# Performance work log

Measured on AMD Instinct MI355X. Metric: run time of the kernel, lower is better.

The kernel has to match this reference:

```python
import jax, jax.numpy as jnp
import numpy as np

NUM_HEADS = 32
HIDDEN = 4096
HEAD_DIM = HIDDEN // NUM_HEADS
BATCH = 1
SEQ = 2048


def setup_inputs() -> dict:
    key = jax.random.key(0)
    ks = jax.random.split(key, 8)
    hidden_states = jax.random.normal(ks[0], (BATCH, SEQ, HIDDEN), dtype=jnp.float32)
    residual = jax.random.normal(ks[1], (BATCH, SEQ, HIDDEN), dtype=jnp.float32)
    # BLOOM alibi: [batch*heads, 1, kv_len], broadcast over q_length in baddbmm
    alibi = jax.random.normal(ks[2], (BATCH * NUM_HEADS, 1, SEQ), dtype=jnp.float32) * 0.1
    # causal boolean mask: True = masked (filled with -inf before softmax)
    attention_mask = ~jnp.tril(jnp.ones((SEQ, SEQ), dtype=bool))[None, None, :, :]
    scale = 0.02
    Wqkv = jax.random.normal(ks[3], (3 * HIDDEN, HIDDEN), dtype=jnp.float32) * scale
    bqkv = jax.random.normal(ks[4], (3 * HIDDEN,), dtype=jnp.float32) * scale
    Wd = jax.random.normal(ks[5], (HIDDEN, HIDDEN), dtype=jnp.float32) * scale
    bd = jax.random.normal(ks[6], (HIDDEN,), dtype=jnp.float32) * scale
    return {"hidden_states": hidden_states, "residual": residual, "alibi": alibi,
            "attention_mask": attention_mask, "Wqkv": Wqkv, "bqkv": bqkv,
            "Wd": Wd, "bd": bd}


def reference(hidden_states, residual, alibi, attention_mask, Wqkv, bqkv, Wd, bd):
    B, S, H = hidden_states.shape
    nh, hd = NUM_HEADS, HEAD_DIM
    inv_norm = 1.0 / np.sqrt(hd).astype(np.float32)

    # fused QKV projection, BLOOM interleaved layout [B, S, nh, 3, hd]
    fused = hidden_states @ Wqkv.T + bqkv           # [B, S, 3H]
    fused = fused.reshape(B, S, nh, 3, hd)
    q = jnp.transpose(fused[..., 0, :], (0, 2, 1, 3))  # [B, nh, S, hd]
    k = jnp.transpose(fused[..., 1, :], (0, 2, 1, 3))  # [B, nh, S, hd]
    v = jnp.transpose(fused[..., 2, :], (0, 2, 1, 3))  # [B, nh, S, hd]

    # baddbmm: alibi + inv_norm * Q @ K^T
    alibi_b = alibi.reshape(B, nh, 1, S)                # broadcast over q_length
    scores = alibi_b + inv_norm * jnp.einsum('bhqd,bhkd->bhqk', q, k)
    scores = jnp.where(attention_mask, jnp.finfo(scores.dtype).min, scores)
    probs = jax.nn.softmax(scores, axis=-1)             # [B, nh, S, S]

    ctx = jnp.einsum('bhqk,bhkd->bhqd', probs, v)       # [B, nh, S, hd]
    ctx = jnp.transpose(ctx, (0, 2, 1, 3)).reshape(B, S, H)
    out = ctx @ Wd.T + bd
    return residual + out
```

## Files before the change

### kernel.cpp

```cpp
#include <hip/hip_runtime.h>


#define SEQL 2048
#define HIDN 4096
#define NHEAD 32
#define HDIM 128
#define H3 12288

typedef __bf16 bf16x8 __attribute__((ext_vector_type(8)));
typedef float f32x4 __attribute__((ext_vector_type(4)));
typedef unsigned short u16x8 __attribute__((ext_vector_type(8)));
typedef unsigned int u32x4 __attribute__((ext_vector_type(4)));

__device__ __forceinline__ unsigned short f2bf(float f) {
  union { float f; unsigned u; } v; v.f = f;
  return (unsigned short)((v.u + 0x7FFFu + ((v.u >> 16) & 1u)) >> 16);
}

__device__ __forceinline__ unsigned cvtpk(float lo, float hi) {
  unsigned r;
  asm("v_cvt_pk_bf16_f32 %0, %1, %2" : "=v"(r) : "v"(lo), "v"(hi));
  return r;
}

__device__ __forceinline__ void gload_lds16(const void* g, void* l) {
  __builtin_amdgcn_global_load_lds(
      (const __attribute__((address_space(1))) void*)g,
      (__attribute__((address_space(3))) void*)l, 16, 0, 0);
}

__global__ __launch_bounds__(256) void cvt_f32_bf16(
    const float* __restrict__ in, unsigned short* __restrict__ out, long long n) {
  long long i = ((long long)blockIdx.x * blockDim.x + threadIdx.x) * 8;
  long long stride = (long long)gridDim.x * blockDim.x * 8;
  for (; i < n; i += stride) {
    float4 a = *(const float4*)(in + i);
    float4 b = *(const float4*)(in + i + 4);
    u16x8 o;
    o[0] = f2bf(a.x); o[1] = f2bf(a.y); o[2] = f2bf(a.z); o[3] = f2bf(a.w);
    o[4] = f2bf(b.x); o[5] = f2bf(b.y); o[6] = f2bf(b.z); o[7] = f2bf(b.w);
    *(u16x8*)(out + i) = o;
  }
}

template <int EPI>
__global__ __launch_bounds__(256) void gemm_nt(
    const unsigned short* __restrict__ A, const unsigned short* __restrict__ B,
    int M, int N, int K,
    const float* __restrict__ bias, const float* __restrict__ residual,
    float* __restrict__ outf,
    unsigned short* __restrict__ q_bf, unsigned short* __restrict__ k_bf,
    unsigned short* __restrict__ v_t) {
  __shared__ unsigned short As[128 * 64];
  __shared__ unsigned short Bs[128 * 64];

  const int tid = threadIdx.x;
  const int l = tid & 63;
  const int w = tid >> 6;
  const int wr = (w >> 1) * 64;
  const int wc = (w & 1) * 64;

  const int nb = gridDim.x;
  const int lin = (blockIdx.x & 7) * (nb >> 3) + (blockIdx.x >> 3);
  const int tm0 = (lin & 15) * 128;
  const int tn0 = (lin >> 4) * 128;

  const int lr = l >> 3;
  const int lc = (l & 7) ^ lr;

  f32x4 acc[4][4] = {};

  for (int kt = 0; kt < K; kt += 64) {
    __syncthreads();
#pragma unroll
    for (int i = 0; i < 4; ++i) {
      const int row = w * 32 + i * 8 + lr;
      gload_lds16(&A[(long long)(tm0 + row) * K + kt + lc * 8],
                  (char*)As + (w * 4 + i) * 1024);
      gload_lds16(&B[(long long)(tn0 + row) * K + kt + lc * 8],
                  (char*)Bs + (w * 4 + i) * 1024);
    }
    __syncthreads();
#pragma unroll
    for (int kk = 0; kk < 2; ++kk) {
      const int colb = kk * 64 + (l >> 4) * 16;
      bf16x8 af[4], bfr[4];
#pragma unroll
      for (int m = 0; m < 4; ++m) {
        int row = wr + m * 16 + (l & 15);
        af[m] = *(const bf16x8*)((char*)As + row * 128 + (colb ^ ((row & 7) << 4)));
      }
#pragma unroll
      for (int n = 0; n < 4; ++n) {
        int row = wc + n * 16 + (l & 15);
        bfr[n] = *(const bf16x8*)((char*)Bs + row * 128 + (colb ^ ((row & 7) << 4)));
      }
#pragma unroll
      for (int m = 0; m < 4; ++m)
#pragma unroll
        for (int n = 0; n < 4; ++n)
          acc[m][n] = __builtin_amdgcn_mfma_f32_16x16x32_bf16(af[m], bfr[n], acc[m][n], 0, 0, 0);
    }
  }

#pragma unroll
  for (int m = 0; m < 4; ++m) {
#pragma unroll
    for (int n = 0; n < 4; ++n) {
      const int col = tn0 + wc + n * 16 + (l & 15);
      const float bv = bias[col];
#pragma unroll
      for (int r = 0; r < 4; ++r) {
        const int rowg = tm0 + wr + m * 16 + (l >> 4) * 4 + r;
        float v = acc[m][n][r] + bv;
        if (EPI == 0) {
          const int head = col / 384;
          const int rem = col - head * 384;
          const int which = rem >> 7;
          const int d = rem & 127;
          const unsigned short bv16 = f2bf(v);
          if (which == 0)
            q_bf[(long long)(head * SEQL + rowg) * HDIM + d] = bv16;
          else if (which == 1)
            k_bf[(long long)(head * SEQL + rowg) * HDIM + d] = bv16;
          else
            v_t[(long long)(head * HDIM + d) * SEQL + rowg] = bv16;
        } else {
          const long long idx = (long long)rowg * N + col;
          outf[idx] = v + residual[idx];
        }
      }
    }
  }
}

__global__ __launch_bounds__(256) void attn_fwd(
    const unsigned short* __restrict__ q_bf, const unsigned short* __restrict__ k_bf,
    const unsigned short* __restrict__ v_t, const float* __restrict__ alibi,
    unsigned short* __restrict__ ctx_bf) {
  __shared__ unsigned short Ks[64 * 128];
  __shared__ unsigned short Vs[128 * 64];
  __shared__ float Al[SEQL];

  const int tid = threadIdx.x;
  const int l = tid & 63;
  const int w = tid >> 6;
  const int q = l & 15;
  const int g = l >> 4;

  const float LOG2E = 1.4426950408889634f;

  const int b = blockIdx.x;
  const int i_ = b >> 3;
  const int h = (b & 7) * 4 + (i_ & 3);
  const int qtile = 31 - (i_ >> 2);
  const int qw = qtile * 64 + w * 16;
  const int qrow = qw + q;
  const int ntiles = qtile + 1;

  for (int i = tid; i < SEQL; i += 256) Al[i] = alibi[h * SEQL + i] * LOG2E;

  bf16x8 qf[4];
  {
    const unsigned short* qp =
        &q_bf[(long long)(h * SEQL + qw + q) * HDIM + g * 8];
#pragma unroll
    for (int kk = 0; kk < 4; ++kk) qf[kk] = *(const bf16x8*)(qp + kk * 32);
  }

  f32x4 oacc[8] = {};
  float mrun = -__builtin_inff();
  float lrun = 0.f;
  const float inv_norm2 = 0.08838834764831845f * 1.4426950408889634f;

  const int kR = l >> 4, kC = l & 15;
  const int vR = l >> 3, vC = (l & 7) ^ vR;

  for (int t = 0; t < ntiles; ++t) {
    const int kv0 = t * 64;
    __syncthreads();
#pragma unroll
    for (int i = 0; i < 4; ++i) {
      const int krow = w * 16 + i * 4 + kR;
      const int ksrc = kC ^ ((i & 1) * 4 + kR);
      gload_lds16(&k_bf[(long long)(h * SEQL + kv0 + krow) * HDIM + ksrc * 8],
                  (char*)Ks + (w * 4 + i) * 1024);
      const int vrow = w * 32 + i * 8 + vR;
      gload_lds16(&v_t[(long long)(h * HDIM + vrow) * SEQL + kv0 + vC * 8],
                  (char*)Vs + (w * 4 + i) * 1024);
    }
    __syncthreads();

    if (kv0 <= qw + 15) {
      f32x4 sacc[4] = {};
#pragma unroll
      for (int kk = 0; kk < 4; ++kk) {
        const int colb = kk * 64 + g * 16;
#pragma unroll
        for (int n = 0; n < 4; ++n) {
          const int row = n * 16 + q;
          bf16x8 kf = *(const bf16x8*)((char*)Ks + row * 256 + (colb ^ ((row & 7) << 4)));
          sacc[n] = __builtin_amdgcn_mfma_f32_16x16x32_bf16(kf, qf[kk], sacc[n], 0, 0, 0);
        }
      }

      float p[4][4];
      float m0 = -__builtin_inff();
#pragma unroll
      for (int n = 0; n < 4; ++n) {
        const f32x4 alv = *(const f32x4*)(Al + kv0 + n * 16 + g * 4);
#pragma unroll
        for (int r = 0; r < 4; ++r) {
          const int kv = kv0 + n * 16 + g * 4 + r;
          float v = alv[r] + inv_norm2 * sacc[n][r];
          v = (kv > qrow) ? -__builtin_inff() : v;
          p[n][r] = v;
          m0 = fmaxf(m0, v);
        }
      }
      m0 = fmaxf(m0, __shfl_xor(m0, 16, 64));
      m0 = fmaxf(m0, __shfl_xor(m0, 32, 64));
      if (__ballot(m0 > mrun + 11.0f)) {
        const float mnew = fmaxf(mrun, m0);
        const float scale = exp2f(mrun - mnew);
        mrun = mnew;
        lrun *= scale;
#pragma unroll
        for (int n2 = 0; n2 < 8; ++n2)
#pragma unroll
          for (int r = 0; r < 4; ++r) oacc[n2][r] *= scale;
      }
      float p0 = 0.f;
#pragma unroll
      for (int n = 0; n < 4; ++n)
#pragma unroll
        for (int r = 0; r < 4; ++r) {
          const float pv = exp2f(p[n][r] - mrun);
          p[n][r] = pv;
          p0 += pv;
        }
      p0 += __shfl_xor(p0, 16, 64);
      p0 += __shfl_xor(p0, 32, 64);
      lrun += p0;

      bf16x8 pb[2];
#pragma unroll
      for (int kk2 = 0; kk2 < 2; ++kk2) {
        const int n0 = 2 * kk2;
        const unsigned pk0 = cvtpk(p[n0][0], p[n0][1]);
        const unsigned pk1 = cvtpk(p[n0][2], p[n0][3]);
        const unsigned pk2 = cvtpk(p[n0 + 1][0], p[n0 + 1][1]);
        const unsigned pk3 = cvtpk(p[n0 + 1][2], p[n0 + 1][3]);
        const int s0 = q + 32 * (g & 1);
        const int s2 = s0 + 16;
        const unsigned a0 = __shfl((int)pk0, s0, 64), b0 = __shfl((int)pk2, s0, 64);
        const unsigned a1 = __shfl((int)pk1, s0, 64), b1 = __shfl((int)pk3, s0, 64);
        const unsigned a2 = __shfl((int)pk0, s2, 64), b2 = __shfl((int)pk2, s2, 64);
        const unsigned a3 = __shfl((int)pk1, s2, 64), b3 = __shfl((int)pk3, s2, 64);
        const bool lo = (g < 2);
        u32x4 wv;
        wv[0] = lo ? a0 : b0; wv[1] = lo ? a1 : b1;
        wv[2] = lo ? a2 : b2; wv[3] = lo ? a3 : b3;
        pb[kk2] = __builtin_bit_cast(bf16x8, wv);
      }

#pragma unroll
      for (int n2 = 0; n2 < 8; ++n2) {
#pragma unroll
        for (int kk2 = 0; kk2 < 2; ++kk2) {
          const int row = n2 * 16 + q;
          const int colb = kk2 * 64 + g * 16;
          bf16x8 vf = *(const bf16x8*)((char*)Vs + row * 128 + (colb ^ ((row & 7) << 4)));
          oacc[n2] = __builtin_amdgcn_mfma_f32_16x16x32_bf16(vf, pb[kk2], oacc[n2], 0, 0, 0);
        }
      }
    }
  }

  __syncthreads();
  {
    char* scr = (char*)Ks + w * 4096;
    const float rdiv = 1.0f / lrun;
#pragma unroll
    for (int n2 = 0; n2 < 8; ++n2)
#pragma unroll
      for (int r = 0; r < 4; ++r) {
        const int d = n2 * 16 + g * 4 + r;
        *(unsigned short*)(scr + ((q * 256 + d * 2) ^ ((q & 7) << 4))) =
            f2bf(oacc[n2][r] * rdiv);
      }
    __threadfence_block();
    const int q2 = l >> 2;
#pragma unroll
    for (int i = 0; i < 4; ++i) {
      const int chunk = (l & 3) + i * 4;
      u16x8 v = *(const u16x8*)(scr + ((q2 * 256 + chunk * 16) ^ ((q2 & 7) << 4)));
      *(u16x8*)&ctx_bf[(long long)(qw + q2) * HIDN + h * HDIM + chunk * 8] = v;
    }
  }
}

extern "C" void kernel_launch(void* const* d_in, const int* in_sizes, int n_in,
                              void* d_out, int out_size, void* d_ws, size_t ws_size,
                              hipStream_t stream) {
  const float* hidden = (const float*)d_in[0];
  const float* residual = (const float*)d_in[1];
  const float* alibi = (const float*)d_in[2];
  const float* Wqkv = (const float*)d_in[4];
  const float* bqkv = (const float*)d_in[5];
  const float* Wd = (const float*)d_in[6];
  const float* bd = (const float*)d_in[7];
  float* out = (float*)d_out;

  char* ws = (char*)d_ws;
  const size_t MB16 = 16777216;
  unsigned short* q_bf = (unsigned short*)(ws);
  unsigned short* k_bf = (unsigned short*)(ws + MB16);
  unsigned short* v_t = (unsigned short*)(ws + 2 * MB16);
  unsigned short* hid_bf = (unsigned short*)(ws + 3 * MB16);
  unsigned short* wqkv_bf = (unsigned short*)(ws + 4 * MB16);
  unsigned short* wd_bf = (unsigned short*)(ws + 4 * MB16);
  unsigned short* ctx_bf = (unsigned short*)(ws + 4 * MB16 + 33554432);

  cvt_f32_bf16<<<4096, 256, 0, stream>>>(hidden, hid_bf, (long long)SEQL * HIDN);
  cvt_f32_bf16<<<24576, 256, 0, stream>>>(Wqkv, wqkv_bf, (long long)H3 * HIDN);

  gemm_nt<0><<<(SEQL / 128) * (H3 / 128), 256, 0, stream>>>(
      hid_bf, wqkv_bf, SEQL, H3, HIDN, bqkv, nullptr, nullptr, q_bf, k_bf, v_t);

  cvt_f32_bf16<<<8192, 256, 0, stream>>>(Wd, wd_bf, (long long)HIDN * HIDN);

  attn_fwd<<<NHEAD * (SEQL / 64), 256, 0, stream>>>(q_bf, k_bf, v_t, alibi, ctx_bf);

  gemm_nt<1><<<(SEQL / 128) * (HIDN / 128), 256, 0, stream>>>(
      ctx_bf, wd_bf, SEQL, HIDN, HIDN, bd, residual, out, nullptr, nullptr, nullptr);
}
```

Before: 475.8 us.

## Process two 16-row query groups per wave to double K/V tile reuse

The attention kernel now assigns 128 query rows per block (32 per wave, as two 16-row groups) instead of 64. Each K/V tile loaded into LDS and each K/V fragment read from LDS feeds twice as many MFMAs, which halves global K/V traffic and the number of barrier-separated loads per unit of work. The cost is more registers per wave (doubled accumulators and Q fragments), which may lower occupancy. It also halves the grid size, which can worsen load balance given the causal triangular work distribution.

```diff
diff --git a/kernel.cpp b/kernel.cpp
--- a/kernel.cpp
+++ b/kernel.cpp
@@ -146,31 +146,31 @@
   const int l = tid & 63;
   const int w = tid >> 6;
   const int q = l & 15;
-  const int g = l >> 4;
+  const int lg = l >> 4;
 
   const float LOG2E = 1.4426950408889634f;
 
   const int b = blockIdx.x;
   const int i_ = b >> 3;
   const int h = (b & 7) * 4 + (i_ & 3);
-  const int qtile = 31 - (i_ >> 2);
-  const int qw = qtile * 64 + w * 16;
-  const int qrow = qw + q;
-  const int ntiles = qtile + 1;
-
-  for (int i = tid; i < SEQL; i += 256) Al[i] = alibi[h * SEQL + i] * LOG2E;
-
-  bf16x8 qf[4];
-  {
+  const int qtile = 15 - (i_ >> 2);
+  const int qw = qtile * 128 + w * 32;
+  const int ntiles = 2 * qtile + 2;
+
+  for (int i = tid; i < ntiles * 64; i += 256) Al[i] = alibi[h * SEQL + i] * LOG2E;
+
+  bf16x8 qf[2][4];
+#pragma unroll
+  for (int g = 0; g < 2; ++g) {
     const unsigned short* qp =
-        &q_bf[(long long)(h * SEQL + qw + q) * HDIM + g * 8];
-#pragma unroll
-    for (int kk = 0; kk < 4; ++kk) qf[kk] = *(const bf16x8*)(qp + kk * 32);
-  }
-
-  f32x4 oacc[8] = {};
-  float mrun = -__builtin_inff();
-  float lrun = 0.f;
+        &q_bf[(long long)(h * SEQL + qw + g * 16 + q) * HDIM + lg * 8];
+#pragma unroll
+    for (int kk = 0; kk < 4; ++kk) qf[g][kk] = *(const bf16x8*)(qp + kk * 32);
+  }
+
+  f32x4 oacc[2][8] = {};
+  float mrun[2] = {-__builtin_inff(), -__builtin_inff()};
+  float lrun[2] = {0.f, 0.f};
   const float inv_norm2 = 0.08838834764831845f * 1.4426950408889634f;
 
   const int kR = l >> 4, kC = l & 15;
@@ -181,87 +181,93 @@
     __syncthreads();
 #pragma unroll
     for (int i = 0; i < 4; ++i) {
-      const int krow = w * 16 + i * 4 + kR;
+      const int c = w * 4 + i;
+      const int krow = c * 4 + kR;
       const int ksrc = kC ^ ((i & 1) * 4 + kR);
       gload_lds16(&k_bf[(long long)(h * SEQL + kv0 + krow) * HDIM + ksrc * 8],
-                  (char*)Ks + (w * 4 + i) * 1024);
-      const int vrow = w * 32 + i * 8 + vR;
+                  (char*)Ks + c * 1024);
+      const int vrow = c * 8 + vR;
       gload_lds16(&v_t[(long long)(h * HDIM + vrow) * SEQL + kv0 + vC * 8],
-                  (char*)Vs + (w * 4 + i) * 1024);
+                  (char*)Vs + c * 1024);
     }
     __syncthreads();
 
-    if (kv0 <= qw + 15) {
-      f32x4 sacc[4] = {};
+    if (kv0 <= qw + 31) {
+      f32x4 sacc[2][4] = {};
 #pragma unroll
       for (int kk = 0; kk < 4; ++kk) {
-        const int colb = kk * 64 + g * 16;
+        const int colb = kk * 64 + lg * 16;
 #pragma unroll
         for (int n = 0; n < 4; ++n) {
           const int row = n * 16 + q;
           bf16x8 kf = *(const bf16x8*)((char*)Ks + row * 256 + (colb ^ ((row & 7) << 4)));
-          sacc[n] = __builtin_amdgcn_mfma_f32_16x16x32_bf16(kf, qf[kk], sacc[n], 0, 0, 0);
-        }
-      }
-
-      float p[4][4];
-      float m0 = -__builtin_inff();
-#pragma unroll
-      for (int n = 0; n < 4; ++n) {
-        const f32x4 alv = *(const f32x4*)(Al + kv0 + n * 16 + g * 4);
-#pragma unroll
-        for (int r = 0; r < 4; ++r) {
-          const int kv = kv0 + n * 16 + g * 4 + r;
-          float v = alv[r] + inv_norm2 * sacc[n][r];
-          v = (kv > qrow) ? -__builtin_inff() : v;
-          p[n][r] = v;
-          m0 = fmaxf(m0, v);
-        }
-      }
-      m0 = fmaxf(m0, __shfl_xor(m0, 16, 64));
-      m0 = fmaxf(m0, __shfl_xor(m0, 32, 64));
-      if (__ballot(m0 > mrun + 11.0f)) {
-        const float mnew = fmaxf(mrun, m0);
-        const float scale = exp2f(mrun - mnew);
-        mrun = mnew;
-        lrun *= scale;
-#pragma unroll
-        for (int n2 = 0; n2 < 8; ++n2)
-#pragma unroll
-          for (int r = 0; r < 4; ++r) oacc[n2][r] *= scale;
-      }
-      float p0 = 0.f;
-#pragma unroll
-      for (int n = 0; n < 4; ++n)
-#pragma unroll
-        for (int r = 0; r < 4; ++r) {
-          const float pv = exp2f(p[n][r] - mrun);
-          p[n][r] = pv;
-          p0 += pv;
-        }
-      p0 += __shfl_xor(p0, 16, 64);
-      p0 += __shfl_xor(p0, 32, 64);
-      lrun += p0;
-
-      bf16x8 pb[2];
-#pragma unroll
-      for (int kk2 = 0; kk2 < 2; ++kk2) {
-        const int n0 = 2 * kk2;
-        const unsigned pk0 = cvtpk(p[n0][0], p[n0][1]);
-        const unsigned pk1 = cvtpk(p[n0][2], p[n0][3]);
-        const unsigned pk2 = cvtpk(p[n0 + 1][0], p[n0 + 1][1]);
-        const unsigned pk3 = cvtpk(p[n0 + 1][2], p[n0 + 1][3]);
-        const int s0 = q + 32 * (g & 1);
-        const int s2 = s0 + 16;
-        const unsigned a0 = __shfl((int)pk0, s0, 64), b0 = __shfl((int)pk2, s0, 64);
-        const unsigned a1 = __shfl((int)pk1, s0, 64), b1 = __shfl((int)pk3, s0, 64);
-        const unsigned a2 = __shfl((int)pk0, s2, 64), b2 = __shfl((int)pk2, s2, 64);
-        const unsigned a3 = __shfl((int)pk1, s2, 64), b3 = __shfl((int)pk3, s2, 64);
-        const bool lo = (g < 2);
-        u32x4 wv;
-        wv[0] = lo ? a0 : b0; wv[1] = lo ? a1 : b1;
-        wv[2] = lo ? a2 : b2; wv[3] = lo ? a3 : b3;
-        pb[kk2] = __builtin_bit_cast(bf16x8, wv);
+          sacc[0][n] = __builtin_amdgcn_mfma_f32_16x16x32_bf16(kf, qf[0][kk], sacc[0][n], 0, 0, 0);
+          sacc[1][n] = __builtin_amdgcn_mfma_f32_16x16x32_bf16(kf, qf[1][kk], sacc[1][n], 0, 0, 0);
+        }
+      }
+
+      bf16x8 pb[2][2];
+#pragma unroll
+      for (int g = 0; g < 2; ++g) {
+        const int qrow = qw + g * 16 + q;
+        float p[4][4];
+        float m0 = -__builtin_inff();
+#pragma unroll
+        for (int n = 0; n < 4; ++n) {
+          const f32x4 alv = *(const f32x4*)(Al + kv0 + n * 16 + lg * 4);
+#pragma unroll
+          for (int r = 0; r < 4; ++r) {
+            const int kv = kv0 + n * 16 + lg * 4 + r;
+            float v = alv[r] + inv_norm2 * sacc[g][n][r];
+            v = (kv > qrow) ? -__builtin_inff() : v;
+            p[n][r] = v;
+            m0 = fmaxf(m0, v);
+          }
+        }
+        m0 = fmaxf(m0, __shfl_xor(m0, 16, 64));
+        m0 = fmaxf(m0, __shfl_xor(m0, 32, 64));
+        if (__ballot(m0 > mrun[g] + 11.0f)) {
+          const float mnew = fmaxf(mrun[g], m0);
+          const float scale = exp2f(mrun[g] - mnew);
+          mrun[g] = mnew;
+          lrun[g] *= scale;
+#pragma unroll
+          for (int n2 = 0; n2 < 8; ++n2)
+#pragma unroll
+            for (int r = 0; r < 4; ++r) oacc[g][n2][r] *= scale;
+        }
+        float p0 = 0.f;
+#pragma unroll
+        for (int n = 0; n < 4; ++n)
+#pragma unroll
+          for (int r = 0; r < 4; ++r) {
+            const float pv = exp2f(p[n][r] - mrun[g]);
+            p[n][r] = pv;
+            p0 += pv;
+          }
+        p0 += __shfl_xor(p0, 16, 64);
+        p0 += __shfl_xor(p0, 32, 64);
+        lrun[g] += p0;
+
+#pragma unroll
+        for (int kk2 = 0; kk2 < 2; ++kk2) {
+          const int n0 = 2 * kk2;
+          const unsigned pk0 = cvtpk(p[n0][0], p[n0][1]);
+          const unsigned pk1 = cvtpk(p[n0][2], p[n0][3]);
+          const unsigned pk2 = cvtpk(p[n0 + 1][0], p[n0 + 1][1]);
+          const unsigned pk3 = cvtpk(p[n0 + 1][2], p[n0 + 1][3]);
+          const int s0 = q + 32 * (lg & 1);
+          const int s2 = s0 + 16;
+          const unsigned a0 = __shfl((int)pk0, s0, 64), b0 = __shfl((int)pk2, s0, 64);
+          const unsigned a1 = __shfl((int)pk1, s0, 64), b1 = __shfl((int)pk3, s0, 64);
+          const unsigned a2 = __shfl((int)pk0, s2, 64), b2 = __shfl((int)pk2, s2, 64);
+          const unsigned a3 = __shfl((int)pk1, s2, 64), b3 = __shfl((int)pk3, s2, 64);
+          const bool lo = (lg < 2);
+          u32x4 wv;
+          wv[0] = lo ? a0 : b0; wv[1] = lo ? a1 : b1;
+          wv[2] = lo ? a2 : b2; wv[3] = lo ? a3 : b3;
+          pb[g][kk2] = __builtin_bit_cast(bf16x8, wv);
+        }
       }
 
 #pragma unroll
@@ -269,9 +275,10 @@
 #pragma unroll
         for (int kk2 = 0; kk2 < 2; ++kk2) {
           const int row = n2 * 16 + q;
-          const int colb = kk2 * 64 + g * 16;
+          const int colb = kk2 * 64 + lg * 16;
           bf16x8 vf = *(const bf16x8*)((char*)Vs + row * 128 + (colb ^ ((row & 7) << 4)));
-          oacc[n2] = __builtin_amdgcn_mfma_f32_16x16x32_bf16(vf, pb[kk2], oacc[n2], 0, 0, 0);
+          oacc[0][n2] = __builtin_amdgcn_mfma_f32_16x16x32_bf16(vf, pb[0][kk2], oacc[0][n2], 0, 0, 0);
+          oacc[1][n2] = __builtin_amdgcn_mfma_f32_16x16x32_bf16(vf, pb[1][kk2], oacc[1][n2], 0, 0, 0);
         }
       }
     }
@@ -280,22 +287,26 @@
   __syncthreads();
   {
     char* scr = (char*)Ks + w * 4096;
-    const float rdiv = 1.0f / lrun;
-#pragma unroll
-    for (int n2 = 0; n2 < 8; ++n2)
-#pragma unroll
-      for (int r = 0; r < 4; ++r) {
-        const int d = n2 * 16 + g * 4 + r;
-        *(unsigned short*)(scr + ((q * 256 + d * 2) ^ ((q & 7) << 4))) =
-            f2bf(oacc[n2][r] * rdiv);
-      }
-    __threadfence_block();
-    const int q2 = l >> 2;
-#pragma unroll
-    for (int i = 0; i < 4; ++i) {
-      const int chunk = (l & 3) + i * 4;
-      u16x8 v = *(const u16x8*)(scr + ((q2 * 256 + chunk * 16) ^ ((q2 & 7) << 4)));
-      *(u16x8*)&ctx_bf[(long long)(qw + q2) * HIDN + h * HDIM + chunk * 8] = v;
+#pragma unroll
+    for (int g = 0; g < 2; ++g) {
+      const float rdiv = 1.0f / lrun[g];
+#pragma unroll
+      for (int n2 = 0; n2 < 8; ++n2)
+#pragma unroll
+        for (int r = 0; r < 4; ++r) {
+          const int d = n2 * 16 + lg * 4 + r;
+          *(unsigned short*)(scr + ((q * 256 + d * 2) ^ ((q & 7) << 4))) =
+              f2bf(oacc[g][n2][r] * rdiv);
+        }
+      __threadfence_block();
+      const int q2 = l >> 2;
+#pragma unroll
+      for (int i = 0; i < 4; ++i) {
+        const int chunk = (l & 3) + i * 4;
+        u16x8 v = *(const u16x8*)(scr + ((q2 * 256 + chunk * 16) ^ ((q2 & 7) << 4)));
+        *(u16x8*)&ctx_bf[(long long)(qw + g * 16 + q2) * HIDN + h * HDIM + chunk * 8] = v;
+      }
+      __threadfence_block();
     }
   }
 }
@@ -330,7 +341,7 @@
 
   cvt_f32_bf16<<<8192, 256, 0, stream>>>(Wd, wd_bf, (long long)HIDN * HIDN);
 
-  attn_fwd<<<NHEAD * (SEQL / 64), 256, 0, stream>>>(q_bf, k_bf, v_t, alibi, ctx_bf);
+  attn_fwd<<<NHEAD * (SEQL / 128), 256, 0, stream>>>(q_bf, k_bf, v_t, alibi, ctx_bf);
 
   gemm_nt<1><<<(SEQL / 128) * (HIDN / 128), 256, 0, stream>>>(
       ctx_bf, wd_bf, SEQL, HIDN, HIDN, bd, residual, out, nullptr, nullptr, nullptr);
```

Result: slower. 495.7 us (+4.2%).
